# Kernel tuning notes

Hardware: AMD Instinct MI355X
Metric: run time of the kernel (lower is better)

## Reference

```python
import jax, jax.numpy as jnp
import numpy as np

RRELU_SLOPE = (1.0 / 8.0 + 1.0 / 3.0) / 2.0  # torch.rrelu eval-mode negative slope

N_NODES, N_EDGES, DIM, N_LAYERS = 10000, 640000, 128, 2


def setup_inputs() -> dict:
    key = jax.random.key(0)
    ks = jax.random.split(key, 7)
    scale = 1.0 / np.sqrt(DIM).astype(np.float32)
    return {
        "node_feats": jax.random.normal(ks[0], (N_NODES, DIM), jnp.float32),
        "edge_feats": jax.random.normal(ks[1], (N_EDGES, DIM), jnp.float32),
        "src": jax.random.randint(ks[2], (N_EDGES,), 0, N_NODES),
        "dst": jax.random.randint(ks[3], (N_EDGES,), 0, N_NODES),
        "W1": jax.random.normal(ks[4], (N_LAYERS, DIM, DIM), jnp.float32) * scale,
        "W2": jax.random.normal(ks[5], (N_LAYERS, DIM, DIM), jnp.float32) * scale,
        "W3": jax.random.normal(ks[6], (N_LAYERS, DIM, DIM), jnp.float32) * scale,
    }


def reference(node_feats, edge_feats, src, dst, W1, W2, W3):
    n_nodes = node_feats.shape[0]
    ones = jnp.ones((src.shape[0],), dtype=node_feats.dtype)
    deg = jax.ops.segment_sum(ones, dst, num_segments=n_nodes)  # in-degrees
    iso = (deg == 0)[:, None]                                   # isolated-node mask
    denom = jnp.maximum(deg, 1.0)[:, None]                      # safe mean divisor

    h = node_feats
    for l in range(W1.shape[0]):
        # per-edge message: linear1(src_h + edge_h)
        msg = (h[src] + edge_feats) @ W1[l]                     # (E, H)
        # mean-aggregate to destination nodes (0 for zero in-degree, as in dgl)
        neigh = jax.ops.segment_sum(msg, dst, num_segments=n_nodes) / denom
        # self-loop message; isolated nodes use linear3 instead of linear2
        self_msg = jnp.where(iso, h @ W3[l], h @ W2[l])
        x = neigh + self_msg
        h = jnp.where(x >= 0, x, RRELU_SLOPE * x)               # rrelu (eval mode)
    return h
```

## Files before the change

kernel.cpp:

```cpp
#include <hip/hip_runtime.h>

#define NN 10000
#define NE 640000
#define CAP 124
#define SLOPE 0.22916666666666666f

typedef float    f2v __attribute__((ext_vector_type(2)));
typedef float    f4v __attribute__((ext_vector_type(4)));
typedef unsigned u2v __attribute__((ext_vector_type(2)));
typedef unsigned u4v __attribute__((ext_vector_type(4)));

__device__ __forceinline__ float blo(unsigned v){ return __uint_as_float(v << 16); }
__device__ __forceinline__ float bhi(unsigned v){ return __uint_as_float(v & 0xffff0000u); }
__device__ __forceinline__ unsigned f2b(float x){
  unsigned u = __float_as_uint(x);
  return (u + 0x7fffu + ((u >> 16) & 1u)) >> 16;
}
__device__ __forceinline__ unsigned pack2(float a, float b){
  return f2b(a) | (f2b(b) << 16);
}
__device__ __forceinline__ float rrelu(float x){ return x >= 0.f ? x : x * SLOPE; }
__device__ __forceinline__ int clampi(int x, int hi){ return x < 0 ? 0 : (x > hi ? hi : x); }

__device__ __forceinline__ int detect_f32(const unsigned short* __restrict__ w1){
  int lane = threadIdx.x & 63;
  unsigned short u = w1[lane];
  int e = (u >> 7) & 0xFF;
  int pass = ((u & 0x7FFF) == 0 || (e >= 100 && e <= 135)) ? 1 : 0;
  unsigned long long b = __ballot(pass);
  return (__popcll(b) < 56) ? 1 : 0;
}

__device__ __forceinline__ float2 ld2(const void* p, long i, int f32){
  if (f32) return ((const float2*)p)[i];
  unsigned v = ((const unsigned*)p)[i];
  return make_float2(blo(v), bhi(v));
}
__device__ __forceinline__ void st2(void* p, long i, float2 v, int f32){
  if (f32) ((float2*)p)[i] = v;
  else ((unsigned*)p)[i] = pack2(v.x, v.y);
}

__global__ __launch_bounds__(256) void k_build(const int* __restrict__ src,
                          const int* __restrict__ dst,
                          int* __restrict__ deg,
                          unsigned* __restrict__ csr_eid,
                          unsigned short* __restrict__ csr_src,
                          const void* __restrict__ nf, unsigned* __restrict__ nfbf,
                          const void* __restrict__ W1, const void* __restrict__ W2,
                          const void* __restrict__ W3, unsigned* __restrict__ wpk,
                          const unsigned short* __restrict__ w1u){
  int f32 = detect_f32(w1u);
  int i = blockIdx.x * 256 + threadIdx.x;
  if (i < 49152){
    float2 v;
    if (i < 8192)       v = ld2(W1, i, f32);
    else if (i < 16384) v = ld2(W2, i - 8192, f32);
    else if (i < 24576) v = ld2(W1, 8192 + (i - 16384), f32);
    else if (i < 32768) v = ld2(W2, 8192 + (i - 24576), f32);
    else if (i < 40960) v = ld2(W3, i - 32768, f32);
    else                v = ld2(W3, 8192 + (i - 40960), f32);
    wpk[i] = pack2(v.x, v.y);
  }
  if (i >= NE) return;
  float2 v = ld2(nf, i, f32);
  nfbf[i] = pack2(v.x, v.y);
  int d = clampi(dst[i], NN - 1);
  int slot = atomicAdd(&deg[d], 1);
  slot = slot > (CAP - 1) ? (CAP - 1) : slot;
  csr_eid[d * CAP + slot] = (unsigned)i;
  csr_src[d * CAP + slot] = (unsigned short)clampi(src[i], NN - 1);
}

__global__ __launch_bounds__(256) void k_fused0(const void* __restrict__ ef,
                          const unsigned* __restrict__ nfbf,
                          const int* __restrict__ deg,
                          const unsigned* __restrict__ csr_eid,
                          const unsigned short* __restrict__ csr_src,
                          unsigned* __restrict__ eagg,
                          const unsigned* __restrict__ wpk,
                          unsigned* __restrict__ h1,
                          const unsigned short* __restrict__ w1u){
  int f32 = detect_f32(w1u);
  __shared__ unsigned sA[4][4][64];
  int wave = threadIdx.x >> 6, lane = threadIdx.x & 63;
  int half = lane >> 5, sl = lane & 31;
  int nb = (blockIdx.x * 4 + wave) * 4;
  const u2v* nf2 = (const u2v*)nfbf;

  for (int j = 0; j < 4; ++j){
    int n = nb + j;
    int cnt = deg[n]; if (cnt > CAP) cnt = CAP;
    int beg = n * CAP, end = beg + cnt;
    float inv = 1.f / fmaxf((float)cnt, 1.f);
    float s0=0.f,s1=0.f,s2=0.f,s3=0.f;
    float h0=0.f,h1v=0.f,h2=0.f,h3=0.f;

    if (f32){
      const f4v* ef4 = (const f4v*)ef;
      int i = beg;
      for (; i + 8 <= end; i += 8){
        uint4   e4 = *(const uint4*)&csr_eid[i + 4 * half];
        ushort4 c4 = *(const ushort4*)&csr_src[i + 4 * half];
        unsigned eid[4] = {e4.x, e4.y, e4.z, e4.w};
        unsigned sc[4]  = {c4.x, c4.y, c4.z, c4.w};
        f4v v[4]; u2v hv[4];
        #pragma unroll
        for (int q = 0; q < 4; q++)
          v[q] = __builtin_nontemporal_load(ef4 + (long)eid[q] * 32 + sl);
        #pragma unroll
        for (int q = 0; q < 4; q++)
          hv[q] = nf2[(long)sc[q] * 32 + sl];
        #pragma unroll
        for (int q = 0; q < 4; q++){
          s0 += v[q].x; s1 += v[q].y; s2 += v[q].z; s3 += v[q].w;
          h0 += blo(hv[q].x); h1v += bhi(hv[q].x);
          h2 += blo(hv[q].y); h3  += bhi(hv[q].y);
        }
      }
      for (; i + 2 <= end; i += 2){
        unsigned eid = csr_eid[i + half];
        unsigned sc  = csr_src[i + half];
        f4v v = __builtin_nontemporal_load(ef4 + (long)eid * 32 + sl);
        u2v hv = nf2[(long)sc * 32 + sl];
        s0 += v.x; s1 += v.y; s2 += v.z; s3 += v.w;
        h0 += blo(hv.x); h1v += bhi(hv.x); h2 += blo(hv.y); h3 += bhi(hv.y);
      }
      if (i < end && half == 0){
        unsigned eid = csr_eid[i];
        unsigned sc  = csr_src[i];
        f4v v = __builtin_nontemporal_load(ef4 + (long)eid * 32 + sl);
        u2v hv = nf2[(long)sc * 32 + sl];
        s0 += v.x; s1 += v.y; s2 += v.z; s3 += v.w;
        h0 += blo(hv.x); h1v += bhi(hv.x); h2 += blo(hv.y); h3 += bhi(hv.y);
      }
    } else {
      const u2v* ef2 = (const u2v*)ef;
      int i = beg;
      for (; i + 8 <= end; i += 8){
        uint4   e4 = *(const uint4*)&csr_eid[i + 4 * half];
        ushort4 c4 = *(const ushort4*)&csr_src[i + 4 * half];
        unsigned eid[4] = {e4.x, e4.y, e4.z, e4.w};
        unsigned sc[4]  = {c4.x, c4.y, c4.z, c4.w};
        u2v v[4], hv[4];
        #pragma unroll
        for (int q = 0; q < 4; q++)
          v[q] = __builtin_nontemporal_load(ef2 + (long)eid[q] * 32 + sl);
        #pragma unroll
        for (int q = 0; q < 4; q++)
          hv[q] = nf2[(long)sc[q] * 32 + sl];
        #pragma unroll
        for (int q = 0; q < 4; q++){
          s0 += blo(v[q].x);  s1 += bhi(v[q].x);
          s2 += blo(v[q].y);  s3 += bhi(v[q].y);
          h0 += blo(hv[q].x); h1v += bhi(hv[q].x);
          h2 += blo(hv[q].y); h3  += bhi(hv[q].y);
        }
      }
      for (; i + 2 <= end; i += 2){
        unsigned eid = csr_eid[i + half];
        unsigned sc  = csr_src[i + half];
        u2v v = __builtin_nontemporal_load(ef2 + (long)eid * 32 + sl);
        u2v hv = nf2[(long)sc * 32 + sl];
        s0 += blo(v.x); s1 += bhi(v.x); s2 += blo(v.y); s3 += bhi(v.y);
        h0 += blo(hv.x); h1v += bhi(hv.x); h2 += blo(hv.y); h3 += bhi(hv.y);
      }
      if (i < end && half == 0){
        unsigned eid = csr_eid[i];
        unsigned sc  = csr_src[i];
        u2v v = __builtin_nontemporal_load(ef2 + (long)eid * 32 + sl);
        u2v hv = nf2[(long)sc * 32 + sl];
        s0 += blo(v.x); s1 += bhi(v.x); s2 += blo(v.y); s3 += bhi(v.y);
        h0 += blo(hv.x); h1v += bhi(hv.x); h2 += blo(hv.y); h3 += bhi(hv.y);
      }
    }
    s0 += __shfl_xor(s0, 32); s1 += __shfl_xor(s1, 32);
    s2 += __shfl_xor(s2, 32); s3 += __shfl_xor(s3, 32);
    h0 += __shfl_xor(h0, 32); h1v += __shfl_xor(h1v, 32);
    h2 += __shfl_xor(h2, 32); h3  += __shfl_xor(h3, 32);
    if (half == 0){
      u2v eo; eo.x = pack2(s0, s1); eo.y = pack2(s2, s3);
      ((u2v*)eagg)[(long)n * 32 + sl] = eo;
      u2v ao; ao.x = pack2((s0 + h0) * inv, (s1 + h1v) * inv);
      ao.y = pack2((s2 + h2) * inv, (s3 + h3) * inv);
      *(u2v*)&sA[wave][j][2 * sl] = ao;
    }
  }

  long hb[4]; float a0[4], a1[4];
  #pragma unroll
  for (int j = 0; j < 4; ++j){ hb[j] = (long)(nb + j) * 64; a0[j] = 0.f; a1[j] = 0.f; }
  const unsigned* wp1 = wpk;
  const unsigned* wp2 = wpk + 8192;
  for (int kk = 0; kk < 64; ++kk){
    unsigned w1a = wp1[(2 * kk) * 64 + lane];
    unsigned w1b = wp1[(2 * kk + 1) * 64 + lane];
    unsigned w2a = wp2[(2 * kk) * 64 + lane];
    unsigned w2b = wp2[(2 * kk + 1) * 64 + lane];
    #pragma unroll
    for (int j = 0; j < 4; ++j){
      unsigned av = sA[wave][j][kk];
      unsigned hv = nfbf[hb[j] + kk];
      float A0 = blo(av), A1 = bhi(av);
      float H0 = blo(hv), H1 = bhi(hv);
      a0[j] += A0 * blo(w1a) + A1 * blo(w1b) + H0 * blo(w2a) + H1 * blo(w2b);
      a1[j] += A0 * bhi(w1a) + A1 * bhi(w1b) + H0 * bhi(w2a) + H1 * bhi(w2b);
    }
  }
  #pragma unroll
  for (int j = 0; j < 4; ++j){
    if (deg[nb + j] == 0){
      const unsigned* wp3 = wpk + 32768;
      float b0 = 0.f, b1 = 0.f;
      for (int kk = 0; kk < 64; ++kk){
        unsigned hv = nfbf[hb[j] + kk];
        unsigned wa = wp3[(2 * kk) * 64 + lane];
        unsigned wb = wp3[(2 * kk + 1) * 64 + lane];
        b0 += blo(hv) * blo(wa) + bhi(hv) * blo(wb);
        b1 += blo(hv) * bhi(wa) + bhi(hv) * bhi(wb);
      }
      a0[j] = b0; a1[j] = b1;
    }
  }
  #pragma unroll
  for (int j = 0; j < 4; ++j)
    h1[hb[j] + lane] = pack2(rrelu(a0[j]), rrelu(a1[j]));
}

__global__ __launch_bounds__(256) void k_fused1(const unsigned* __restrict__ h1,
                          const int* __restrict__ deg,
                          const unsigned short* __restrict__ csr_src,
                          const unsigned* __restrict__ eagg,
                          const unsigned* __restrict__ wpk,
                          void* __restrict__ out,
                          const unsigned short* __restrict__ w1u){
  int f32 = detect_f32(w1u);
  __shared__ unsigned sA[4][4][64];
  int wave = threadIdx.x >> 6, lane = threadIdx.x & 63;
  int qt = lane >> 4, ql = lane & 15;
  int nb = (blockIdx.x * 4 + wave) * 4;
  const u4v* h4 = (const u4v*)h1;

  for (int j = 0; j < 4; ++j){
    int n = nb + j;
    int cnt = deg[n]; if (cnt > CAP) cnt = CAP;
    int beg = n * CAP, end = beg + cnt;
    float a0=0.f,a1=0.f,a2=0.f,a3=0.f,a4=0.f,a5=0.f,a6=0.f,a7=0.f;
    int i = beg;
    for (; i + 16 <= end; i += 16){
      ushort4 c4 = *(const ushort4*)&csr_src[i + 4 * qt];
      unsigned sc[4] = {c4.x, c4.y, c4.z, c4.w};
      u4v v[4];
      #pragma unroll
      for (int q = 0; q < 4; q++) v[q] = h4[(long)sc[q] * 16 + ql];
      #pragma unroll
      for (int q = 0; q < 4; q++){
        a0 += blo(v[q].x); a1 += bhi(v[q].x); a2 += blo(v[q].y); a3 += bhi(v[q].y);
        a4 += blo(v[q].z); a5 += bhi(v[q].z); a6 += blo(v[q].w); a7 += bhi(v[q].w);
      }
    }
    for (; i + 4 <= end; i += 4){
      unsigned c = csr_src[i + qt];
      u4v v = h4[(long)c * 16 + ql];
      a0 += blo(v.x); a1 += bhi(v.x); a2 += blo(v.y); a3 += bhi(v.y);
      a4 += blo(v.z); a5 += bhi(v.z); a6 += blo(v.w); a7 += bhi(v.w);
    }
    int r = end - i;
    if (qt < r){
      unsigned c = csr_src[i + qt];
      u4v v = h4[(long)c * 16 + ql];
      a0 += blo(v.x); a1 += bhi(v.x); a2 += blo(v.y); a3 += bhi(v.y);
      a4 += blo(v.z); a5 += bhi(v.z); a6 += blo(v.w); a7 += bhi(v.w);
    }
    a0 += __shfl_xor(a0, 16); a1 += __shfl_xor(a1, 16);
    a2 += __shfl_xor(a2, 16); a3 += __shfl_xor(a3, 16);
    a4 += __shfl_xor(a4, 16); a5 += __shfl_xor(a5, 16);
    a6 += __shfl_xor(a6, 16); a7 += __shfl_xor(a7, 16);
    a0 += __shfl_xor(a0, 32); a1 += __shfl_xor(a1, 32);
    a2 += __shfl_xor(a2, 32); a3 += __shfl_xor(a3, 32);
    a4 += __shfl_xor(a4, 32); a5 += __shfl_xor(a5, 32);
    a6 += __shfl_xor(a6, 32); a7 += __shfl_xor(a7, 32);
    if (qt == 0){
      u4v ev = ((const u4v*)eagg)[(long)n * 16 + ql];
      a0 += blo(ev.x); a1 += bhi(ev.x); a2 += blo(ev.y); a3 += bhi(ev.y);
      a4 += blo(ev.z); a5 += bhi(ev.z); a6 += blo(ev.w); a7 += bhi(ev.w);
      float inv = 1.f / fmaxf((float)cnt, 1.f);
      u4v ao;
      ao.x = pack2(a0 * inv, a1 * inv); ao.y = pack2(a2 * inv, a3 * inv);
      ao.z = pack2(a4 * inv, a5 * inv); ao.w = pack2(a6 * inv, a7 * inv);
      *(u4v*)&sA[wave][j][4 * ql] = ao;
    }
  }

  long hb[4]; float a0[4], a1[4];
  #pragma unroll
  for (int j = 0; j < 4; ++j){ hb[j] = (long)(nb + j) * 64; a0[j] = 0.f; a1[j] = 0.f; }
  const unsigned* wp1 = wpk + 16384;
  const unsigned* wp2 = wpk + 24576;
  for (int kk = 0; kk < 64; ++kk){
    unsigned w1a = wp1[(2 * kk) * 64 + lane];
    unsigned w1b = wp1[(2 * kk + 1) * 64 + lane];
    unsigned w2a = wp2[(2 * kk) * 64 + lane];
    unsigned w2b = wp2[(2 * kk + 1) * 64 + lane];
    #pragma unroll
    for (int j = 0; j < 4; ++j){
      unsigned av = sA[wave][j][kk];
      unsigned hv = h1[hb[j] + kk];
      float A0 = blo(av), A1 = bhi(av);
      float H0 = blo(hv), H1 = bhi(hv);
      a0[j] += A0 * blo(w1a) + A1 * blo(w1b) + H0 * blo(w2a) + H1 * blo(w2b);
      a1[j] += A0 * bhi(w1a) + A1 * bhi(w1b) + H0 * bhi(w2a) + H1 * bhi(w2b);
    }
  }
  #pragma unroll
  for (int j = 0; j < 4; ++j){
    if (deg[nb + j] == 0){
      const unsigned* wp3 = wpk + 40960;
      float b0 = 0.f, b1 = 0.f;
      for (int kk = 0; kk < 64; ++kk){
        unsigned hv = h1[hb[j] + kk];
        unsigned wa = wp3[(2 * kk) * 64 + lane];
        unsigned wb = wp3[(2 * kk + 1) * 64 + lane];
        b0 += blo(hv) * blo(wa) + bhi(hv) * blo(wb);
        b1 += blo(hv) * bhi(wa) + bhi(hv) * bhi(wb);
      }
      a0[j] = b0; a1[j] = b1;
    }
  }
  #pragma unroll
  for (int j = 0; j < 4; ++j)
    st2(out, hb[j] + lane, make_float2(rrelu(a0[j]), rrelu(a1[j])), f32);
}

extern "C" void kernel_launch(void* const* d_in, const int* in_sizes, int n_in,
                              void* d_out, int out_size, void* d_ws, size_t ws_size,
                              hipStream_t stream) {
  const void* nf  = d_in[0];
  const void* ef  = d_in[1];
  const int*  src = (const int*)d_in[2];
  const int*  dst = (const int*)d_in[3];
  const void* W1  = d_in[4];
  const void* W2  = d_in[5];
  const void* W3  = d_in[6];

  char* w = (char*)d_ws;
  int* deg                 = (int*)(w);
  unsigned* csr_eid        = (unsigned*)(w + 40064);
  unsigned short* csr_src  = (unsigned short*)(w + 5000064);
  unsigned* eagg           = (unsigned*)(w + 7480064);
  unsigned* wpk            = (unsigned*)(w + 10040064);
  unsigned* nfbf           = (unsigned*)(w + 10236672);
  unsigned* h1             = (unsigned*)(w + 12796672);

  const unsigned short* w1u = (const unsigned short*)W1;

  hipMemsetAsync(deg, 0, NN * sizeof(int), stream);
  k_build<<<2500, 256, 0, stream>>>(src, dst, deg, csr_eid, csr_src,
                                    nf, nfbf, W1, W2, W3, wpk, w1u);
  k_fused0<<<625, 256, 0, stream>>>(ef, nfbf, deg, csr_eid, csr_src,
                                    eagg, wpk, h1, w1u);
  k_fused1<<<625, 256, 0, stream>>>(h1, deg, csr_src, eagg, wpk, d_out, w1u);
}
```

Baseline: 561.7 us.

## Replace scalar dense projection with bf16 MFMA using prepacked weight fragments

Both fused kernels now compute the per-node W1/W2 projection with 16x16x32 bf16 MFMA instructions over a 16-node tile per block, replacing a scalar FMA loop per wave. The build kernel repacks W1/W2 into MFMA B-fragment layout, and the aggregated and self features are staged in XOR-swizzled shared memory to avoid bank conflicts. The isolated-node W3 path stays scalar and overwrites the output after a barrier. This adds block-level syncs and relies on the correct ordering between the MFMA store and the W3 overwrite.

```diff
diff --git a/kernel.cpp b/kernel.cpp
--- a/kernel.cpp
+++ b/kernel.cpp
@@ -5,10 +5,11 @@
 #define CAP 124
 #define SLOPE 0.22916666666666666f
 
-typedef float    f2v __attribute__((ext_vector_type(2)));
-typedef float    f4v __attribute__((ext_vector_type(4)));
-typedef unsigned u2v __attribute__((ext_vector_type(2)));
-typedef unsigned u4v __attribute__((ext_vector_type(4)));
+typedef float    f4v  __attribute__((ext_vector_type(4)));
+typedef unsigned u2v  __attribute__((ext_vector_type(2)));
+typedef unsigned u4v  __attribute__((ext_vector_type(4)));
+typedef short    s8v  __attribute__((ext_vector_type(8)));
+typedef float    f32x4 __attribute__((ext_vector_type(4)));
 
 __device__ __forceinline__ float blo(unsigned v){ return __uint_as_float(v << 16); }
 __device__ __forceinline__ float bhi(unsigned v){ return __uint_as_float(v & 0xffff0000u); }
@@ -40,6 +41,10 @@
   if (f32) ((float2*)p)[i] = v;
   else ((unsigned*)p)[i] = pack2(v.x, v.y);
 }
+__device__ __forceinline__ unsigned welem(const void* W, long idx, int f32){
+  if (f32) return f2b(((const float*)W)[idx]);
+  return ((const unsigned short*)W)[idx];
+}
 
 __global__ __launch_bounds__(256) void k_build(const int* __restrict__ src,
                           const int* __restrict__ dst,
@@ -48,19 +53,32 @@
                           unsigned short* __restrict__ csr_src,
                           const void* __restrict__ nf, unsigned* __restrict__ nfbf,
                           const void* __restrict__ W1, const void* __restrict__ W2,
-                          const void* __restrict__ W3, unsigned* __restrict__ wpk,
+                          const void* __restrict__ W3,
+                          unsigned* __restrict__ wfrag, unsigned* __restrict__ w3pk,
                           const unsigned short* __restrict__ w1u){
   int f32 = detect_f32(w1u);
   int i = blockIdx.x * 256 + threadIdx.x;
-  if (i < 49152){
-    float2 v;
-    if (i < 8192)       v = ld2(W1, i, f32);
-    else if (i < 16384) v = ld2(W2, i - 8192, f32);
-    else if (i < 24576) v = ld2(W1, 8192 + (i - 16384), f32);
-    else if (i < 32768) v = ld2(W2, 8192 + (i - 24576), f32);
-    else if (i < 40960) v = ld2(W3, i - 32768, f32);
-    else                v = ld2(W3, 8192 + (i - 40960), f32);
-    wpk[i] = pack2(v.x, v.y);
+  if (i < 32768){
+    int L = i >> 14, f = i & 16383;
+    int kt = f >> 11, rem = f & 2047;
+    int nt = rem >> 8, rem2 = rem & 255;
+    int ln = rem2 >> 2, pj = rem2 & 3;
+    int k0 = kt * 32 + ((ln >> 4) << 3) + 2 * pj;
+    int n  = nt * 16 + (ln & 15);
+    long base = (long)L * 16384;
+    unsigned lo, hi;
+    if (kt < 4){
+      lo = welem(W1, base + (long)k0 * 128 + n, f32);
+      hi = welem(W1, base + (long)(k0 + 1) * 128 + n, f32);
+    } else {
+      lo = welem(W2, base + (long)(k0 - 128) * 128 + n, f32);
+      hi = welem(W2, base + (long)(k0 - 127) * 128 + n, f32);
+    }
+    wfrag[i] = lo | (hi << 16);
+  } else if (i < 49152){
+    int ii = i - 32768;
+    float2 v = ld2(W3, ii, f32);
+    w3pk[ii] = pack2(v.x, v.y);
   }
   if (i >= NE) return;
   float2 v = ld2(nf, i, f32);
@@ -78,18 +96,29 @@
                           const unsigned* __restrict__ csr_eid,
                           const unsigned short* __restrict__ csr_src,
                           unsigned* __restrict__ eagg,
-                          const unsigned* __restrict__ wpk,
+                          const unsigned* __restrict__ wfrag,
+                          const unsigned* __restrict__ w3pk,
                           unsigned* __restrict__ h1,
                           const unsigned short* __restrict__ w1u){
   int f32 = detect_f32(w1u);
-  __shared__ unsigned sA[4][4][64];
+  __shared__ unsigned sA[16][64];
+  __shared__ unsigned sH[16][64];
   int wave = threadIdx.x >> 6, lane = threadIdx.x & 63;
   int half = lane >> 5, sl = lane & 31;
-  int nb = (blockIdx.x * 4 + wave) * 4;
+  int nb = blockIdx.x * 16;
+  char* sAb = (char*)&sA[0][0];
+  char* sHb = (char*)&sH[0][0];
+
+  {
+    int row = threadIdx.x >> 4, ch = threadIdx.x & 15;
+    u4v hv = ((const u4v*)nfbf)[(long)(nb + row) * 16 + ch];
+    *(u4v*)(sHb + row * 256 + ((ch * 16) ^ ((row & 7) << 4))) = hv;
+  }
+
   const u2v* nf2 = (const u2v*)nfbf;
-
   for (int j = 0; j < 4; ++j){
-    int n = nb + j;
+    int row = wave * 4 + j;
+    int n = nb + row;
     int cnt = deg[n]; if (cnt > CAP) cnt = CAP;
     int beg = n * CAP, end = beg + cnt;
     float inv = 1.f / fmaxf((float)cnt, 1.f);
@@ -183,66 +212,78 @@
       ((u2v*)eagg)[(long)n * 32 + sl] = eo;
       u2v ao; ao.x = pack2((s0 + h0) * inv, (s1 + h1v) * inv);
       ao.y = pack2((s2 + h2) * inv, (s3 + h3) * inv);
-      *(u2v*)&sA[wave][j][2 * sl] = ao;
-    }
-  }
-
-  long hb[4]; float a0[4], a1[4];
+      *(u2v*)(sAb + row * 256 + ((sl * 8) ^ ((row & 7) << 4))) = ao;
+    }
+  }
+  __syncthreads();
+
+  int m = lane & 15, g = lane >> 4;
+  int nt0 = wave * 2, nt1 = nt0 + 1;
+  f32x4 acc0 = {0.f,0.f,0.f,0.f}, acc1 = {0.f,0.f,0.f,0.f};
+  const char* wf = (const char*)wfrag;
   #pragma unroll
-  for (int j = 0; j < 4; ++j){ hb[j] = (long)(nb + j) * 64; a0[j] = 0.f; a1[j] = 0.f; }
-  const unsigned* wp1 = wpk;
-  const unsigned* wp2 = wpk + 8192;
-  for (int kk = 0; kk < 64; ++kk){
-    unsigned w1a = wp1[(2 * kk) * 64 + lane];
-    unsigned w1b = wp1[(2 * kk + 1) * 64 + lane];
-    unsigned w2a = wp2[(2 * kk) * 64 + lane];
-    unsigned w2b = wp2[(2 * kk + 1) * 64 + lane];
-    #pragma unroll
-    for (int j = 0; j < 4; ++j){
-      unsigned av = sA[wave][j][kk];
-      unsigned hv = nfbf[hb[j] + kk];
-      float A0 = blo(av), A1 = bhi(av);
-      float H0 = blo(hv), H1 = bhi(hv);
-      a0[j] += A0 * blo(w1a) + A1 * blo(w1b) + H0 * blo(w2a) + H1 * blo(w2b);
-      a1[j] += A0 * bhi(w1a) + A1 * bhi(w1b) + H0 * bhi(w2a) + H1 * bhi(w2b);
-    }
-  }
+  for (int kt = 0; kt < 8; ++kt){
+    const char* basep = (kt < 4) ? sAb : sHb;
+    int kb = (kt & 3) * 64 + g * 16;
+    s8v a = *(const s8v*)(basep + m * 256 + (kb ^ ((m & 7) << 4)));
+    s8v b0 = *(const s8v*)(wf + (((kt * 8 + nt0) * 64 + lane) << 4));
+    s8v b1 = *(const s8v*)(wf + (((kt * 8 + nt1) * 64 + lane) << 4));
+    acc0 = __builtin_amdgcn_mfma_f32_16x16x32_bf16(a, b0, acc0, 0, 0, 0);
+    acc1 = __builtin_amdgcn_mfma_f32_16x16x32_bf16(a, b1, acc1, 0, 0, 0);
+  }
+  unsigned short* h1s = (unsigned short*)h1;
+  #pragma unroll
+  for (int r = 0; r < 4; ++r){
+    long node = nb + g * 4 + r;
+    h1s[node * 128 + nt0 * 16 + m] = (unsigned short)f2b(rrelu(acc0[r]));
+    h1s[node * 128 + nt1 * 16 + m] = (unsigned short)f2b(rrelu(acc1[r]));
+  }
+  __syncthreads();
+
   #pragma unroll
   for (int j = 0; j < 4; ++j){
-    if (deg[nb + j] == 0){
-      const unsigned* wp3 = wpk + 32768;
+    int n = nb + wave * 4 + j;
+    if (deg[n] == 0){
       float b0 = 0.f, b1 = 0.f;
       for (int kk = 0; kk < 64; ++kk){
-        unsigned hv = nfbf[hb[j] + kk];
-        unsigned wa = wp3[(2 * kk) * 64 + lane];
-        unsigned wb = wp3[(2 * kk + 1) * 64 + lane];
+        unsigned hv = nfbf[(long)n * 64 + kk];
+        unsigned wa = w3pk[(2 * kk) * 64 + lane];
+        unsigned wb = w3pk[(2 * kk + 1) * 64 + lane];
         b0 += blo(hv) * blo(wa) + bhi(hv) * blo(wb);
         b1 += blo(hv) * bhi(wa) + bhi(hv) * bhi(wb);
       }
-      a0[j] = b0; a1[j] = b1;
-    }
-  }
-  #pragma unroll
-  for (int j = 0; j < 4; ++j)
-    h1[hb[j] + lane] = pack2(rrelu(a0[j]), rrelu(a1[j]));
+      h1[(long)n * 64 + lane] = pack2(rrelu(b0), rrelu(b1));
+    }
+  }
 }
 
 __global__ __launch_bounds__(256) void k_fused1(const unsigned* __restrict__ h1,
                           const int* __restrict__ deg,
                           const unsigned short* __restrict__ csr_src,
                           const unsigned* __restrict__ eagg,
-                          const unsigned* __restrict__ wpk,
+                          const unsigned* __restrict__ wfrag,
+                          const unsigned* __restrict__ w3pk,
                           void* __restrict__ out,
                           const unsigned short* __restrict__ w1u){
   int f32 = detect_f32(w1u);
-  __shared__ unsigned sA[4][4][64];
+  __shared__ unsigned sA[16][64];
+  __shared__ unsigned sH[16][64];
   int wave = threadIdx.x >> 6, lane = threadIdx.x & 63;
   int qt = lane >> 4, ql = lane & 15;
-  int nb = (blockIdx.x * 4 + wave) * 4;
+  int nb = blockIdx.x * 16;
+  char* sAb = (char*)&sA[0][0];
+  char* sHb = (char*)&sH[0][0];
   const u4v* h4 = (const u4v*)h1;
 
+  {
+    int row = threadIdx.x >> 4, ch = threadIdx.x & 15;
+    u4v hv = h4[(long)(nb + row) * 16 + ch];
+    *(u4v*)(sHb + row * 256 + ((ch * 16) ^ ((row & 7) << 4))) = hv;
+  }
+
   for (int j = 0; j < 4; ++j){
-    int n = nb + j;
+    int row = wave * 4 + j;
+    int n = nb + row;
     int cnt = deg[n]; if (cnt > CAP) cnt = CAP;
     int beg = n * CAP, end = beg + cnt;
     float a0=0.f,a1=0.f,a2=0.f,a3=0.f,a4=0.f,a5=0.f,a6=0.f,a7=0.f;
@@ -288,48 +329,60 @@
       u4v ao;
       ao.x = pack2(a0 * inv, a1 * inv); ao.y = pack2(a2 * inv, a3 * inv);
       ao.z = pack2(a4 * inv, a5 * inv); ao.w = pack2(a6 * inv, a7 * inv);
-      *(u4v*)&sA[wave][j][4 * ql] = ao;
-    }
-  }
-
-  long hb[4]; float a0[4], a1[4];
+      *(u4v*)(sAb + row * 256 + ((ql * 16) ^ ((row & 7) << 4))) = ao;
+    }
+  }
+  __syncthreads();
+
+  int m = lane & 15, g = lane >> 4;
+  int nt0 = wave * 2, nt1 = nt0 + 1;
+  f32x4 acc0 = {0.f,0.f,0.f,0.f}, acc1 = {0.f,0.f,0.f,0.f};
+  const char* wf = (const char*)(wfrag + 16384);
   #pragma unroll
-  for (int j = 0; j < 4; ++j){ hb[j] = (long)(nb + j) * 64; a0[j] = 0.f; a1[j] = 0.f; }
-  const unsigned* wp1 = wpk + 16384;
-  const unsigned* wp2 = wpk + 24576;
-  for (int kk = 0; kk < 64; ++kk){
-    unsigned w1a = wp1[(2 * kk) * 64 + lane];
-    unsigned w1b = wp1[(2 * kk + 1) * 64 + lane];
-    unsigned w2a = wp2[(2 * kk) * 64 + lane];
-    unsigned w2b = wp2[(2 * kk + 1) * 64 + lane];
+  for (int kt = 0; kt < 8; ++kt){
+    const char* basep = (kt < 4) ? sAb : sHb;
+    int kb = (kt & 3) * 64 + g * 16;
+    s8v a = *(const s8v*)(basep + m * 256 + (kb ^ ((m & 7) << 4)));
+    s8v b0 = *(const s8v*)(wf + (((kt * 8 + nt0) * 64 + lane) << 4));
+    s8v b1 = *(const s8v*)(wf + (((kt * 8 + nt1) * 64 + lane) << 4));
+    acc0 = __builtin_amdgcn_mfma_f32_16x16x32_bf16(a, b0, acc0, 0, 0, 0);
+    acc1 = __builtin_amdgcn_mfma_f32_16x16x32_bf16(a, b1, acc1, 0, 0, 0);
+  }
+  if (f32){
+    float* of = (float*)out;
     #pragma unroll
-    for (int j = 0; j < 4; ++j){
-      unsigned av = sA[wave][j][kk];
-      unsigned hv = h1[hb[j] + kk];
-      float A0 = blo(av), A1 = bhi(av);
-      float H0 = blo(hv), H1 = bhi(hv);
-      a0[j] += A0 * blo(w1a) + A1 * blo(w1b) + H0 * blo(w2a) + H1 * blo(w2b);
-      a1[j] += A0 * bhi(w1a) + A1 * bhi(w1b) + H0 * bhi(w2a) + H1 * bhi(w2b);
-    }
-  }
+    for (int r = 0; r < 4; ++r){
+      long node = nb + g * 4 + r;
+      of[node * 128 + nt0 * 16 + m] = rrelu(acc0[r]);
+      of[node * 128 + nt1 * 16 + m] = rrelu(acc1[r]);
+    }
+  } else {
+    unsigned short* os = (unsigned short*)out;
+    #pragma unroll
+    for (int r = 0; r < 4; ++r){
+      long node = nb + g * 4 + r;
+      os[node * 128 + nt0 * 16 + m] = (unsigned short)f2b(rrelu(acc0[r]));
+      os[node * 128 + nt1 * 16 + m] = (unsigned short)f2b(rrelu(acc1[r]));
+    }
+  }
+  __syncthreads();
+
   #pragma unroll
   for (int j = 0; j < 4; ++j){
-    if (deg[nb + j] == 0){
-      const unsigned* wp3 = wpk + 40960;
+    int n = nb + wave * 4 + j;
+    if (deg[n] == 0){
+      const unsigned* wp3 = w3pk + 8192;
       float b0 = 0.f, b1 = 0.f;
       for (int kk = 0; kk < 64; ++kk){
-        unsigned hv = h1[hb[j] + kk];
+        unsigned hv = h1[(long)n * 64 + kk];
         unsigned wa = wp3[(2 * kk) * 64 + lane];
         unsigned wb = wp3[(2 * kk + 1) * 64 + lane];
         b0 += blo(hv) * blo(wa) + bhi(hv) * blo(wb);
         b1 += blo(hv) * bhi(wa) + bhi(hv) * bhi(wb);
       }
-      a0[j] = b0; a1[j] = b1;
-    }
-  }
-  #pragma unroll
-  for (int j = 0; j < 4; ++j)
-    st2(out, hb[j] + lane, make_float2(rrelu(a0[j]), rrelu(a1[j])), f32);
+      st2(out, (long)n * 64 + lane, make_float2(rrelu(b0), rrelu(b1)), f32);
+    }
+  }
 }
 
 extern "C" void kernel_launch(void* const* d_in, const int* in_sizes, int n_in,
@@ -348,7 +401,8 @@
   unsigned* csr_eid        = (unsigned*)(w + 40064);
   unsigned short* csr_src  = (unsigned short*)(w + 5000064);
   unsigned* eagg           = (unsigned*)(w + 7480064);
-  unsigned* wpk            = (unsigned*)(w + 10040064);
+  unsigned* wfrag          = (unsigned*)(w + 10040064);
+  unsigned* w3pk           = (unsigned*)(w + 10171136);
   unsigned* nfbf           = (unsigned*)(w + 10236672);
   unsigned* h1             = (unsigned*)(w + 12796672);
 
@@ -356,8 +410,9 @@
 
   hipMemsetAsync(deg, 0, NN * sizeof(int), stream);
   k_build<<<2500, 256, 0, stream>>>(src, dst, deg, csr_eid, csr_src,
-                                    nf, nfbf, W1, W2, W3, wpk, w1u);
+                                    nf, nfbf, W1, W2, W3, wfrag, w3pk, w1u);
   k_fused0<<<625, 256, 0, stream>>>(ef, nfbf, deg, csr_eid, csr_src,
-                                    eagg, wpk, h1, w1u);
-  k_fused1<<<625, 256, 0, stream>>>(h1, deg, csr_src, eagg, wpk, d_out, w1u);
-}
+                                    eagg, wfrag, w3pk, h1, w1u);
+  k_fused1<<<625, 256, 0, stream>>>(h1, deg, csr_src, eagg, wfrag, w3pk,
+                                    d_out, w1u);
+}
```

New measurement: 519.7 us. -7.5%, faster.
